# Kernel optimization log

Measured on AMD Instinct MI355X. Metric: run time of the kernel, lower is better.

## Reference

```python
import jax, jax.numpy as jnp
import numpy as np

B, T, C, H, F = 4, 1024, 1024, 16, 4096
D = C // H

def _ln(x, g, b):
    m = x.mean(-1, keepdims=True)
    v = ((x - m) ** 2).mean(-1, keepdims=True)
    return (x - m) * jax.lax.rsqrt(v + 1e-5) * g + b

def setup_inputs() -> dict:
    key = jax.random.key(0)
    ks = jax.random.split(key, 9)
    p = lambda k, shape: jax.random.normal(k, shape, jnp.float32) * 0.02
    return dict(
        x=jax.random.normal(ks[0], (B, T, C), jnp.float32),
        context=jax.random.normal(ks[1], (B, T, C), jnp.float32),
        ln1_g=jnp.ones((C,), jnp.float32), ln1_b=jnp.zeros((C,), jnp.float32),
        qkv_w=p(ks[2], (C, 3 * C)), qkv_b=jnp.zeros((3 * C,), jnp.float32),
        attn_out_w=p(ks[3], (C, C)), attn_out_b=jnp.zeros((C,), jnp.float32),
        lnc_g=jnp.ones((C,), jnp.float32), lnc_b=jnp.zeros((C,), jnp.float32),
        q_w=p(ks[4], (C, C)), q_b=jnp.zeros((C,), jnp.float32),
        kv_w=p(ks[5], (C, 2 * C)), kv_b=jnp.zeros((2 * C,), jnp.float32),
        cross_out_w=p(ks[6], (C, C)), cross_out_b=jnp.zeros((C,), jnp.float32),
        ln2_g=jnp.ones((C,), jnp.float32), ln2_b=jnp.zeros((C,), jnp.float32),
        ffn_w1=p(ks[7], (C, F)), ffn_b1=jnp.zeros((F,), jnp.float32),
        ffn_w2=p(ks[8], (F, C)), ffn_b2=jnp.zeros((C,), jnp.float32),
    )

def reference(x, context, ln1_g, ln1_b, qkv_w, qkv_b, attn_out_w, attn_out_b,
              lnc_g, lnc_b, q_w, q_b, kv_w, kv_b, cross_out_w, cross_out_b,
              ln2_g, ln2_b, ffn_w1, ffn_b1, ffn_w2, ffn_b2):
    scale = 1.0 / np.sqrt(D)
    # --- causal self-attention ---
    h = _ln(x, ln1_g, ln1_b)
    qkv = (h @ qkv_w + qkv_b).reshape(B, T, 3, H, D)
    q, k, v = qkv[:, :, 0], qkv[:, :, 1], qkv[:, :, 2]  # [B,T,H,D]
    s = jnp.einsum('bqhd,bkhd->bhqk', q, k) * scale     # [B,H,T,T]
    causal = jnp.tril(jnp.ones((T, T), bool))
    s = jnp.where(causal, s, -jnp.inf)
    a = jax.nn.softmax(s, axis=-1)
    o = jnp.einsum('bhqk,bkhd->bqhd', a, v).reshape(B, T, C)
    x = x + o @ attn_out_w + attn_out_b
    # --- cross-attention (query=x, context=encoder) ---
    h = _ln(x, lnc_g, lnc_b)
    q = (h @ q_w + q_b).reshape(B, T, H, D)
    kv = (context @ kv_w + kv_b).reshape(B, T, 2, H, D)
    k, v = kv[:, :, 0], kv[:, :, 1]
    s = jnp.einsum('bqhd,bkhd->bhqk', q, k) * scale
    a = jax.nn.softmax(s, axis=-1)
    o = jnp.einsum('bhqk,bkhd->bqhd', a, v).reshape(B, T, C)
    x = x + o @ cross_out_w + cross_out_b
    # --- FFN (exact GELU as in torch default) ---
    h = _ln(x, ln2_g, ln2_b)
    h = jax.nn.gelu(h @ ffn_w1 + ffn_b1, approximate=False)
    return x + h @ ffn_w2 + ffn_b2
```

## Files before the change

### kernel.cpp

```cpp
#include <hip/hip_runtime.h>
#include <hip/hip_bf16.h>

#define BT 4096
#define TT 1024
#define HN 16

typedef __attribute__((ext_vector_type(8))) short bf16x8;
typedef __attribute__((ext_vector_type(4))) float f32x4;

__device__ __forceinline__ unsigned short f2bf(float f) {
    unsigned u = __builtin_bit_cast(unsigned, f);
    unsigned r = (u + 0x7fffu + ((u >> 16) & 1u)) >> 16;
    return (unsigned short)r;
}

__device__ __forceinline__ void g2l16(const void* g, void* l) {
    __builtin_amdgcn_global_load_lds(
        (__attribute__((address_space(1))) void*)(g),
        (__attribute__((address_space(3))) void*)(l), 16, 0, 0);
}

__global__ __launch_bounds__(256)
void transpose_cast(const float* __restrict__ W, unsigned short* __restrict__ Wt,
                    int K, int N)
{
    __shared__ float tile[32][33];
    int n0 = blockIdx.x * 32, k0 = blockIdx.y * 32;
    int tx = threadIdx.x, ty = threadIdx.y;
#pragma unroll
    for (int i = ty; i < 32; i += 8)
        tile[i][tx] = W[(size_t)(k0 + i) * N + n0 + tx];
    __syncthreads();
#pragma unroll
    for (int i = ty; i < 32; i += 8)
        Wt[(size_t)(n0 + i) * K + k0 + tx] = f2bf(tile[tx][i]);
}

__global__ __launch_bounds__(256)
void transpose_v(const unsigned short* __restrict__ v, unsigned short* __restrict__ vt,
                 int stride)
{
    __shared__ unsigned short tile[32][33];
    int d0 = blockIdx.x * 32, t0 = blockIdx.y * 32, bh = blockIdx.z;
    int b = bh >> 4, h = bh & 15;
    int tx = threadIdx.x, ty = threadIdx.y;
#pragma unroll
    for (int i = ty; i < 32; i += 8)
        tile[i][tx] = v[((size_t)b * TT + t0 + i) * stride + h * 64 + d0 + tx];
    __syncthreads();
#pragma unroll
    for (int i = ty; i < 32; i += 8)
        vt[((size_t)bh * 64 + d0 + i) * TT + t0 + tx] = tile[tx][i];
}

__global__ __launch_bounds__(256)
void cast_bf16(const float* __restrict__ in, unsigned short* __restrict__ out)
{
    int i = blockIdx.x * 256 + threadIdx.x;
    float4 v = ((const float4*)in)[i];
    ushort4 o;
    o.x = f2bf(v.x); o.y = f2bf(v.y); o.z = f2bf(v.z); o.w = f2bf(v.w);
    ((ushort4*)out)[i] = o;
}

__global__ __launch_bounds__(256)
void ln_kernel(const float* __restrict__ x, const float* __restrict__ g,
               const float* __restrict__ bta, unsigned short* __restrict__ out)
{
    __shared__ float red[8];
    int row = blockIdx.x;
    const float* xr = x + (size_t)row * 1024;
    float4 v = ((const float4*)xr)[threadIdx.x];
    float s = v.x + v.y + v.z + v.w;
    float q = v.x*v.x + v.y*v.y + v.z*v.z + v.w*v.w;
#pragma unroll
    for (int m = 1; m < 64; m <<= 1) {
        s += __shfl_xor(s, m, 64);
        q += __shfl_xor(q, m, 64);
    }
    int wave = threadIdx.x >> 6;
    if ((threadIdx.x & 63) == 0) { red[wave] = s; red[4 + wave] = q; }
    __syncthreads();
    s = red[0] + red[1] + red[2] + red[3];
    q = red[4] + red[5] + red[6] + red[7];
    float mean = s * (1.f / 1024.f);
    float var  = q * (1.f / 1024.f) - mean * mean;
    float rstd = rsqrtf(var + 1e-5f);
    float4 gv = ((const float4*)g)[threadIdx.x];
    float4 bv = ((const float4*)bta)[threadIdx.x];
    ushort4 o;
    o.x = f2bf((v.x - mean) * rstd * gv.x + bv.x);
    o.y = f2bf((v.y - mean) * rstd * gv.y + bv.y);
    o.z = f2bf((v.z - mean) * rstd * gv.z + bv.z);
    o.w = f2bf((v.w - mean) * rstd * gv.w + bv.w);
    ((ushort4*)(out + (size_t)row * 1024))[threadIdx.x] = o;
}

template<int MODE>
__global__ __launch_bounds__(256)
void gemm_bt(const unsigned short* __restrict__ A,
             const unsigned short* __restrict__ Bt,
             const float* __restrict__ bias,
             const float* __restrict__ res,
             void* __restrict__ outp,
             int M, int N, int K)
{
    __shared__ unsigned short lA[128 * 64];
    __shared__ unsigned short lB[128 * 64];
    const int tid = threadIdx.x;
    const int wave = tid >> 6, lane = tid & 63;
    const int quad = lane >> 4, l16 = lane & 15;
    const int m0 = blockIdx.y * 128, n0 = blockIdx.x * 128;
    const int wrow = (wave >> 1) * 64, wcol = (wave & 1) * 64;

    f32x4 acc[4][4];
#pragma unroll
    for (int i = 0; i < 4; ++i)
#pragma unroll
        for (int j = 0; j < 4; ++j)
#pragma unroll
            for (int r = 0; r < 4; ++r) acc[i][j][r] = 0.f;

    for (int k0 = 0; k0 < K; k0 += 64) {
        __syncthreads();
#pragma unroll
        for (int it = 0; it < 4; ++it) {
            int chunk = it * 256 + tid;
            int row = chunk >> 3, kc = chunk & 7;
            g2l16(A  + (size_t)(m0 + row) * K + k0 + kc * 8, &lA[chunk * 8]);
            g2l16(Bt + (size_t)(n0 + row) * K + k0 + kc * 8, &lB[chunk * 8]);
        }
        __syncthreads();
#pragma unroll
        for (int kk = 0; kk < 64; kk += 32) {
            bf16x8 af[4], bfr[4];
#pragma unroll
            for (int i = 0; i < 4; ++i)
                af[i] = *(const bf16x8*)&lA[(wrow + i * 16 + l16) * 64 + kk + quad * 8];
#pragma unroll
            for (int j = 0; j < 4; ++j)
                bfr[j] = *(const bf16x8*)&lB[(wcol + j * 16 + l16) * 64 + kk + quad * 8];
#pragma unroll
            for (int i = 0; i < 4; ++i)
#pragma unroll
                for (int j = 0; j < 4; ++j)
                    acc[i][j] = __builtin_amdgcn_mfma_f32_16x16x32_bf16(af[i], bfr[j], acc[i][j], 0, 0, 0);
        }
    }

#pragma unroll
    for (int i = 0; i < 4; ++i) {
#pragma unroll
        for (int r = 0; r < 4; ++r) {
            int m = m0 + wrow + i * 16 + quad * 4 + r;
#pragma unroll
            for (int j = 0; j < 4; ++j) {
                int n = n0 + wcol + j * 16 + l16;
                float v = acc[i][j][r] + bias[n];
                if (MODE == 1) v = 0.5f * v * (1.f + erff(v * 0.70710678118654752f));
                size_t idx = (size_t)m * N + n;
                if (MODE == 2) ((float*)outp)[idx] = v + res[idx];
                else ((unsigned short*)outp)[idx] = f2bf(v);
            }
        }
    }
}

__global__ __launch_bounds__(256)
void attn_kernel(const unsigned short* __restrict__ qp,
                 const unsigned short* __restrict__ kp,
                 const unsigned short* __restrict__ vt,
                 unsigned short* __restrict__ op,
                 int qstride, int kstride, int causal)
{
    __shared__ unsigned short lK[64 * 72];
    __shared__ unsigned short lV[64 * 72];
    __shared__ unsigned short lP[4][16 * 72];

    const int tid = threadIdx.x;
    const int wave = tid >> 6, lane = tid & 63;
    const int quad = lane >> 4, l16 = lane & 15;
    const int bh = blockIdx.y, b = bh >> 4, h = bh & 15;
    const int qtile = causal ? (gridDim.x - 1 - blockIdx.x) : blockIdx.x;
    const int q0 = qtile * 64;
    const size_t rowbase = (size_t)b * TT;
    const int hoff = h * 64;
    const unsigned short* vbase = vt + (size_t)bh * 64 * TT;

    bf16x8 qf[2];
    {
        int qrow = q0 + wave * 16 + l16;
        const unsigned short* qrp = qp + (rowbase + qrow) * (size_t)qstride + hoff;
        qf[0] = *(const bf16x8*)(qrp + quad * 8);
        qf[1] = *(const bf16x8*)(qrp + 32 + quad * 8);
    }

    f32x4 oacc[4];
#pragma unroll
    for (int jd = 0; jd < 4; ++jd)
#pragma unroll
        for (int r = 0; r < 4; ++r) oacc[jd][r] = 0.f;
    float mrun = -1e30f, lrun = 0.f;

    const int nkt = causal ? (qtile + 1) : (TT / 64);
    for (int kt = 0; kt < nkt; ++kt) {
        __syncthreads();
#pragma unroll
        for (int it = 0; it < 2; ++it) {
            int c = it * 256 + tid;
            int r8 = c >> 3, cc = c & 7;
            *(bf16x8*)&lK[r8 * 72 + cc * 8] =
                *(const bf16x8*)(kp + (rowbase + kt * 64 + r8) * (size_t)kstride + hoff + cc * 8);
            *(bf16x8*)&lV[r8 * 72 + cc * 8] =
                *(const bf16x8*)(vbase + (size_t)r8 * TT + kt * 64 + cc * 8);
        }
        __syncthreads();

        f32x4 s[4];
#pragma unroll
        for (int i = 0; i < 4; ++i)
#pragma unroll
            for (int r = 0; r < 4; ++r) s[i][r] = 0.f;
#pragma unroll
        for (int kk = 0; kk < 2; ++kk) {
            bf16x8 kf[4];
#pragma unroll
            for (int i = 0; i < 4; ++i)
                kf[i] = *(const bf16x8*)&lK[(i * 16 + l16) * 72 + kk * 32 + quad * 8];
#pragma unroll
            for (int i = 0; i < 4; ++i)
                s[i] = __builtin_amdgcn_mfma_f32_16x16x32_bf16(kf[i], qf[kk], s[i], 0, 0, 0);
        }

        const int qg = q0 + wave * 16 + l16;
        const bool domask = (causal != 0) && (kt == qtile);
        float mloc = -1e30f;
#pragma unroll
        for (int i = 0; i < 4; ++i)
#pragma unroll
            for (int r = 0; r < 4; ++r) {
                float v = s[i][r] * 0.125f;
                if (domask) {
                    int kg = kt * 64 + i * 16 + quad * 4 + r;
                    if (kg > qg) v = -1e30f;
                }
                s[i][r] = v;
                mloc = fmaxf(mloc, v);
            }
        mloc = fmaxf(mloc, __shfl_xor(mloc, 16, 64));
        mloc = fmaxf(mloc, __shfl_xor(mloc, 32, 64));
        float mn = fmaxf(mrun, mloc);
        float alpha = __expf(mrun - mn);
        mrun = mn;
        float ls = 0.f;
#pragma unroll
        for (int i = 0; i < 4; ++i)
#pragma unroll
            for (int r = 0; r < 4; ++r) {
                float p = __expf(s[i][r] - mn);
                s[i][r] = p;
                ls += p;
            }
        ls += __shfl_xor(ls, 16, 64);
        ls += __shfl_xor(ls, 32, 64);
        lrun = lrun * alpha + ls;

        float arow[4];
#pragma unroll
        for (int r = 0; r < 4; ++r)
            arow[r] = __shfl(alpha, quad * 4 + r, 64);
#pragma unroll
        for (int jd = 0; jd < 4; ++jd)
#pragma unroll
            for (int r = 0; r < 4; ++r) oacc[jd][r] *= arow[r];

        unsigned short* pw = lP[wave];
#pragma unroll
        for (int i = 0; i < 4; ++i) {
            ushort4 pk;
            pk.x = f2bf(s[i][0]); pk.y = f2bf(s[i][1]);
            pk.z = f2bf(s[i][2]); pk.w = f2bf(s[i][3]);
            *(ushort4*)&pw[l16 * 72 + i * 16 + quad * 4] = pk;
        }

#pragma unroll
        for (int kk = 0; kk < 2; ++kk) {
            bf16x8 pf = *(const bf16x8*)&pw[l16 * 72 + kk * 32 + quad * 8];
            bf16x8 vf[4];
#pragma unroll
            for (int jd = 0; jd < 4; ++jd)
                vf[jd] = *(const bf16x8*)&lV[(jd * 16 + l16) * 72 + kk * 32 + quad * 8];
#pragma unroll
            for (int jd = 0; jd < 4; ++jd)
                oacc[jd] = __builtin_amdgcn_mfma_f32_16x16x32_bf16(pf, vf[jd], oacc[jd], 0, 0, 0);
        }
    }

    float ir[4];
#pragma unroll
    for (int r = 0; r < 4; ++r)
        ir[r] = 1.f / __shfl(lrun, quad * 4 + r, 64);
#pragma unroll
    for (int r = 0; r < 4; ++r) {
        int qg = q0 + wave * 16 + quad * 4 + r;
        unsigned short* orow = op + (rowbase + qg) * (size_t)1024 + hoff;
#pragma unroll
        for (int jd = 0; jd < 4; ++jd)
            orow[jd * 16 + l16] = f2bf(oacc[jd][r] * ir[r]);
    }
}

extern "C" void kernel_launch(void* const* d_in, const int* in_sizes, int n_in,
                              void* d_out, int out_size, void* d_ws, size_t ws_size,
                              hipStream_t stream)
{
    const float* x     = (const float*)d_in[0];
    const float* ctx   = (const float*)d_in[1];
    const float* ln1_g = (const float*)d_in[2];
    const float* ln1_b = (const float*)d_in[3];
    const float* qkv_w = (const float*)d_in[4];
    const float* qkv_b = (const float*)d_in[5];
    const float* aow   = (const float*)d_in[6];
    const float* aob   = (const float*)d_in[7];
    const float* lnc_g = (const float*)d_in[8];
    const float* lnc_b = (const float*)d_in[9];
    const float* q_w   = (const float*)d_in[10];
    const float* q_b   = (const float*)d_in[11];
    const float* kv_w  = (const float*)d_in[12];
    const float* kv_b  = (const float*)d_in[13];
    const float* cow   = (const float*)d_in[14];
    const float* cob   = (const float*)d_in[15];
    const float* ln2_g = (const float*)d_in[16];
    const float* ln2_b = (const float*)d_in[17];
    const float* f1w   = (const float*)d_in[18];
    const float* f1b   = (const float*)d_in[19];
    const float* f2w   = (const float*)d_in[20];
    const float* f2b   = (const float*)d_in[21];

    char* ws = (char*)d_ws;
    size_t off = 0;
    auto alloc = [&](size_t bytes) {
        char* p = ws + off;
        off += (bytes + 255) & ~(size_t)255;
        return p;
    };

    unsigned short* WtQKV = (unsigned short*)alloc((size_t)3072 * 1024 * 2);
    unsigned short* WtAO  = (unsigned short*)alloc((size_t)1024 * 1024 * 2);
    unsigned short* WtQ   = (unsigned short*)alloc((size_t)1024 * 1024 * 2);
    unsigned short* WtKV  = (unsigned short*)alloc((size_t)2048 * 1024 * 2);
    unsigned short* WtCO  = (unsigned short*)alloc((size_t)1024 * 1024 * 2);
    unsigned short* WtF1  = (unsigned short*)alloc((size_t)4096 * 1024 * 2);
    unsigned short* WtF2  = (unsigned short*)alloc((size_t)1024 * 4096 * 2);
    unsigned short* hA    = (unsigned short*)alloc((size_t)BT * 1024 * 2);
    unsigned short* ctxb  = (unsigned short*)alloc((size_t)BT * 1024 * 2);
    unsigned short* qkvb  = (unsigned short*)alloc((size_t)BT * 3072 * 2);
    unsigned short* o1    = (unsigned short*)alloc((size_t)BT * 1024 * 2);
    float*          x1    = (float*)alloc((size_t)BT * 1024 * 4);
    unsigned short* qb    = (unsigned short*)alloc((size_t)BT * 1024 * 2);
    unsigned short* kvb   = (unsigned short*)alloc((size_t)BT * 2048 * 2);
    unsigned short* o2    = (unsigned short*)alloc((size_t)BT * 1024 * 2);
    float*          x2    = (float*)alloc((size_t)BT * 1024 * 4);
    unsigned short* mid   = (unsigned short*)alloc((size_t)BT * 4096 * 2);
    unsigned short* vT1   = (unsigned short*)alloc((size_t)BT * 1024 * 2);
    unsigned short* vT2   = (unsigned short*)alloc((size_t)BT * 1024 * 2);

    dim3 tb(32, 8);
    transpose_cast<<<dim3(3072/32, 1024/32), tb, 0, stream>>>(qkv_w, WtQKV, 1024, 3072);
    transpose_cast<<<dim3(1024/32, 1024/32), tb, 0, stream>>>(aow,   WtAO,  1024, 1024);
    transpose_cast<<<dim3(1024/32, 1024/32), tb, 0, stream>>>(q_w,   WtQ,   1024, 1024);
    transpose_cast<<<dim3(2048/32, 1024/32), tb, 0, stream>>>(kv_w,  WtKV,  1024, 2048);
    transpose_cast<<<dim3(1024/32, 1024/32), tb, 0, stream>>>(cow,   WtCO,  1024, 1024);
    transpose_cast<<<dim3(4096/32, 1024/32), tb, 0, stream>>>(f1w,   WtF1,  1024, 4096);
    transpose_cast<<<dim3(1024/32, 4096/32), tb, 0, stream>>>(f2w,   WtF2,  4096, 1024);

    cast_bf16<<<BT * 1024 / 4 / 256, 256, 0, stream>>>(ctx, ctxb);

    ln_kernel<<<BT, 256, 0, stream>>>(x, ln1_g, ln1_b, hA);
    gemm_bt<0><<<dim3(3072/128, BT/128), 256, 0, stream>>>(hA, WtQKV, qkv_b, nullptr, qkvb, BT, 3072, 1024);
    transpose_v<<<dim3(2, TT/32, 64), tb, 0, stream>>>(qkvb + 2048, vT1, 3072);
    attn_kernel<<<dim3(TT/64, 64), 256, 0, stream>>>(qkvb, qkvb + 1024, vT1, o1, 3072, 3072, 1);
    gemm_bt<2><<<dim3(1024/128, BT/128), 256, 0, stream>>>(o1, WtAO, aob, x, x1, BT, 1024, 1024);

    ln_kernel<<<BT, 256, 0, stream>>>(x1, lnc_g, lnc_b, hA);
    gemm_bt<0><<<dim3(1024/128, BT/128), 256, 0, stream>>>(hA, WtQ, q_b, nullptr, qb, BT, 1024, 1024);
    gemm_bt<0><<<dim3(2048/128, BT/128), 256, 0, stream>>>(ctxb, WtKV, kv_b, nullptr, kvb, BT, 2048, 1024);
    transpose_v<<<dim3(2, TT/32, 64), tb, 0, stream>>>(kvb + 1024, vT2, 2048);
    attn_kernel<<<dim3(TT/64, 64), 256, 0, stream>>>(qb, kvb, vT2, o2, 1024, 2048, 0);
    gemm_bt<2><<<dim3(1024/128, BT/128), 256, 0, stream>>>(o2, WtCO, cob, x1, x2, BT, 1024, 1024);

    ln_kernel<<<BT, 256, 0, stream>>>(x2, ln2_g, ln2_b, hA);
    gemm_bt<1><<<dim3(4096/128, BT/128), 256, 0, stream>>>(hA, WtF1, f1b, nullptr, mid, BT, 4096, 1024);
    gemm_bt<2><<<dim3(1024/128, BT/128), 256, 0, stream>>>(mid, WtF2, f2b, x2, (float*)d_out, BT, 1024, 4096);
}
```

Before: 620.2 us.

## Batch weight transposes, merge Q/KV GEMMs, add split-K and smaller-tile GEMMs

Replaces seven weight transpose launches with one table-driven kernel. Merges the cross-attention Q and KV projections into a single dual-GEMM launch. Uses 64-row tiles for the N=1024 output projections so the grid has more blocks. Splits the K=4096 FFN down-projection four ways into fp32 partials, reusing the qkv scratch region, then sums them with bias and residual in a separate reduction kernel. Together these aim to raise CU utilisation on undersized grids and cut launch overhead, at the cost of extra partial-sum memory traffic and reliance on the allocator placing the scratch buffers contiguously.

```diff
diff --git a/kernel.cpp b/kernel.cpp
--- a/kernel.cpp
+++ b/kernel.cpp
@@ -20,12 +20,28 @@
         (__attribute__((address_space(3))) void*)(l), 16, 0, 0);
 }
 
-__global__ __launch_bounds__(256)
-void transpose_cast(const float* __restrict__ W, unsigned short* __restrict__ Wt,
-                    int K, int N)
+struct TransJobs {
+    const float* W[7];
+    unsigned short* Wt[7];
+    int K[7], N[7];
+    int start[8];
+};
+
+__global__ __launch_bounds__(256)
+void transpose_all(TransJobs J)
 {
     __shared__ float tile[32][33];
-    int n0 = blockIdx.x * 32, k0 = blockIdx.y * 32;
+    int bx = blockIdx.x;
+    int j = 0;
+#pragma unroll
+    for (int t = 0; t < 7; ++t)
+        if (bx >= J.start[t + 1]) j = t + 1;
+    int t = bx - J.start[j];
+    int K = J.K[j], N = J.N[j];
+    int ntx = N >> 5;
+    int n0 = (t % ntx) * 32, k0 = (t / ntx) * 32;
+    const float* W = J.W[j];
+    unsigned short* Wt = J.Wt[j];
     int tx = threadIdx.x, ty = threadIdx.y;
 #pragma unroll
     for (int i = ty; i < 32; i += 8)
@@ -97,6 +113,76 @@
 }
 
 template<int MODE>
+__device__ __forceinline__
+void gemm_core(unsigned short* lA, unsigned short* lB,
+               const unsigned short* __restrict__ A,
+               const unsigned short* __restrict__ Bt,
+               const float* __restrict__ bias,
+               const float* __restrict__ res,
+               void* __restrict__ outp,
+               int N, int K, int m0, int n0, int kbeg, int kend)
+{
+    const int tid = threadIdx.x;
+    const int wave = tid >> 6, lane = tid & 63;
+    const int quad = lane >> 4, l16 = lane & 15;
+    const int wrow = (wave >> 1) * 64, wcol = (wave & 1) * 64;
+
+    f32x4 acc[4][4];
+#pragma unroll
+    for (int i = 0; i < 4; ++i)
+#pragma unroll
+        for (int j = 0; j < 4; ++j)
+#pragma unroll
+            for (int r = 0; r < 4; ++r) acc[i][j][r] = 0.f;
+
+    for (int k0 = kbeg; k0 < kend; k0 += 64) {
+        __syncthreads();
+#pragma unroll
+        for (int it = 0; it < 4; ++it) {
+            int chunk = it * 256 + tid;
+            int row = chunk >> 3, kc = chunk & 7;
+            g2l16(A  + (size_t)(m0 + row) * K + k0 + kc * 8, &lA[chunk * 8]);
+            g2l16(Bt + (size_t)(n0 + row) * K + k0 + kc * 8, &lB[chunk * 8]);
+        }
+        __syncthreads();
+#pragma unroll
+        for (int kk = 0; kk < 64; kk += 32) {
+            bf16x8 af[4], bfr[4];
+#pragma unroll
+            for (int i = 0; i < 4; ++i)
+                af[i] = *(const bf16x8*)&lA[(wrow + i * 16 + l16) * 64 + kk + quad * 8];
+#pragma unroll
+            for (int j = 0; j < 4; ++j)
+                bfr[j] = *(const bf16x8*)&lB[(wcol + j * 16 + l16) * 64 + kk + quad * 8];
+#pragma unroll
+            for (int i = 0; i < 4; ++i)
+#pragma unroll
+                for (int j = 0; j < 4; ++j)
+                    acc[i][j] = __builtin_amdgcn_mfma_f32_16x16x32_bf16(af[i], bfr[j], acc[i][j], 0, 0, 0);
+        }
+    }
+
+#pragma unroll
+    for (int i = 0; i < 4; ++i) {
+#pragma unroll
+        for (int r = 0; r < 4; ++r) {
+            int m = m0 + wrow + i * 16 + quad * 4 + r;
+#pragma unroll
+            for (int j = 0; j < 4; ++j) {
+                int n = n0 + wcol + j * 16 + l16;
+                float v = acc[i][j][r];
+                if (MODE != 3) v += bias[n];
+                if (MODE == 1) v = 0.5f * v * (1.f + erff(v * 0.70710678118654752f));
+                size_t idx = (size_t)m * N + n;
+                if (MODE == 2) ((float*)outp)[idx] = v + res[idx];
+                else if (MODE == 3) ((float*)outp)[idx] = v;
+                else ((unsigned short*)outp)[idx] = f2bf(v);
+            }
+        }
+    }
+}
+
+template<int MODE>
 __global__ __launch_bounds__(256)
 void gemm_bt(const unsigned short* __restrict__ A,
              const unsigned short* __restrict__ Bt,
@@ -107,15 +193,80 @@
 {
     __shared__ unsigned short lA[128 * 64];
     __shared__ unsigned short lB[128 * 64];
+    gemm_core<MODE>(lA, lB, A, Bt, bias, res, outp, N, K,
+                    blockIdx.y * 128, blockIdx.x * 128, 0, K);
+}
+
+__global__ __launch_bounds__(256)
+void gemm_dual(const unsigned short* __restrict__ A1, const unsigned short* __restrict__ B1,
+               const float* __restrict__ b1, unsigned short* __restrict__ o1p, int N1, int nbx1,
+               const unsigned short* __restrict__ A2, const unsigned short* __restrict__ B2,
+               const float* __restrict__ b2, unsigned short* __restrict__ o2p, int N2,
+               int K)
+{
+    __shared__ unsigned short lA[128 * 64];
+    __shared__ unsigned short lB[128 * 64];
+    int bx = blockIdx.x;
+    if (bx < nbx1)
+        gemm_core<0>(lA, lB, A1, B1, b1, nullptr, o1p, N1, K,
+                     blockIdx.y * 128, bx * 128, 0, K);
+    else
+        gemm_core<0>(lA, lB, A2, B2, b2, nullptr, o2p, N2, K,
+                     blockIdx.y * 128, (bx - nbx1) * 128, 0, K);
+}
+
+__global__ __launch_bounds__(256)
+void gemm_splitk(const unsigned short* __restrict__ A,
+                 const unsigned short* __restrict__ Bt,
+                 float* __restrict__ part,
+                 int M, int N, int K, int kslice)
+{
+    __shared__ unsigned short lA[128 * 64];
+    __shared__ unsigned short lB[128 * 64];
+    int kz = blockIdx.z;
+    gemm_core<3>(lA, lB, A, Bt, nullptr, nullptr,
+                 part + (size_t)kz * M * N, N, K,
+                 blockIdx.y * 128, blockIdx.x * 128,
+                 kz * kslice, (kz + 1) * kslice);
+}
+
+__global__ __launch_bounds__(256)
+void reduce4(const float* __restrict__ part, const float* __restrict__ bias,
+             const float* __restrict__ res, float* __restrict__ out, int MN)
+{
+    int i = blockIdx.x * 256 + threadIdx.x;
+    const float4* p = (const float4*)part;
+    int q = MN >> 2;
+    float4 a = p[i], b = p[i + q], c = p[i + 2 * q], d = p[i + 3 * q];
+    float4 bs = ((const float4*)bias)[i & 255];
+    float4 rr = ((const float4*)res)[i];
+    float4 o;
+    o.x = a.x + b.x + c.x + d.x + bs.x + rr.x;
+    o.y = a.y + b.y + c.y + d.y + bs.y + rr.y;
+    o.z = a.z + b.z + c.z + d.z + bs.z + rr.z;
+    o.w = a.w + b.w + c.w + d.w + bs.w + rr.w;
+    ((float4*)out)[i] = o;
+}
+
+__global__ __launch_bounds__(256)
+void gemm_small2(const unsigned short* __restrict__ A,
+                 const unsigned short* __restrict__ Bt,
+                 const float* __restrict__ bias,
+                 const float* __restrict__ res,
+                 float* __restrict__ outp,
+                 int M, int N, int K)
+{
+    __shared__ unsigned short lA[64 * 64];
+    __shared__ unsigned short lB[128 * 64];
     const int tid = threadIdx.x;
     const int wave = tid >> 6, lane = tid & 63;
     const int quad = lane >> 4, l16 = lane & 15;
-    const int m0 = blockIdx.y * 128, n0 = blockIdx.x * 128;
-    const int wrow = (wave >> 1) * 64, wcol = (wave & 1) * 64;
-
-    f32x4 acc[4][4];
-#pragma unroll
-    for (int i = 0; i < 4; ++i)
+    const int m0 = blockIdx.y * 64, n0 = blockIdx.x * 128;
+    const int wrow = (wave >> 1) * 32, wcol = (wave & 1) * 64;
+
+    f32x4 acc[2][4];
+#pragma unroll
+    for (int i = 0; i < 2; ++i)
 #pragma unroll
         for (int j = 0; j < 4; ++j)
 #pragma unroll
@@ -124,24 +275,29 @@
     for (int k0 = 0; k0 < K; k0 += 64) {
         __syncthreads();
 #pragma unroll
-        for (int it = 0; it < 4; ++it) {
+        for (int it = 0; it < 6; ++it) {
             int chunk = it * 256 + tid;
-            int row = chunk >> 3, kc = chunk & 7;
-            g2l16(A  + (size_t)(m0 + row) * K + k0 + kc * 8, &lA[chunk * 8]);
-            g2l16(Bt + (size_t)(n0 + row) * K + k0 + kc * 8, &lB[chunk * 8]);
+            if (chunk < 512) {
+                int row = chunk >> 3, kc = chunk & 7;
+                g2l16(A + (size_t)(m0 + row) * K + k0 + kc * 8, &lA[chunk * 8]);
+            } else {
+                int cb = chunk - 512;
+                int row = cb >> 3, kc = cb & 7;
+                g2l16(Bt + (size_t)(n0 + row) * K + k0 + kc * 8, &lB[cb * 8]);
+            }
         }
         __syncthreads();
 #pragma unroll
         for (int kk = 0; kk < 64; kk += 32) {
-            bf16x8 af[4], bfr[4];
-#pragma unroll
-            for (int i = 0; i < 4; ++i)
+            bf16x8 af[2], bfr[4];
+#pragma unroll
+            for (int i = 0; i < 2; ++i)
                 af[i] = *(const bf16x8*)&lA[(wrow + i * 16 + l16) * 64 + kk + quad * 8];
 #pragma unroll
             for (int j = 0; j < 4; ++j)
                 bfr[j] = *(const bf16x8*)&lB[(wcol + j * 16 + l16) * 64 + kk + quad * 8];
 #pragma unroll
-            for (int i = 0; i < 4; ++i)
+            for (int i = 0; i < 2; ++i)
 #pragma unroll
                 for (int j = 0; j < 4; ++j)
                     acc[i][j] = __builtin_amdgcn_mfma_f32_16x16x32_bf16(af[i], bfr[j], acc[i][j], 0, 0, 0);
@@ -149,18 +305,15 @@
     }
 
 #pragma unroll
-    for (int i = 0; i < 4; ++i) {
+    for (int i = 0; i < 2; ++i) {
 #pragma unroll
         for (int r = 0; r < 4; ++r) {
             int m = m0 + wrow + i * 16 + quad * 4 + r;
 #pragma unroll
             for (int j = 0; j < 4; ++j) {
                 int n = n0 + wcol + j * 16 + l16;
-                float v = acc[i][j][r] + bias[n];
-                if (MODE == 1) v = 0.5f * v * (1.f + erff(v * 0.70710678118654752f));
                 size_t idx = (size_t)m * N + n;
-                if (MODE == 2) ((float*)outp)[idx] = v + res[idx];
-                else ((unsigned short*)outp)[idx] = f2bf(v);
+                outp[idx] = acc[i][j][r] + bias[n] + res[idx];
             }
         }
     }
@@ -365,31 +518,43 @@
     unsigned short* vT1   = (unsigned short*)alloc((size_t)BT * 1024 * 2);
     unsigned short* vT2   = (unsigned short*)alloc((size_t)BT * 1024 * 2);
 
+    float* partials = (float*)qkvb;
+
+    TransJobs J;
+    J.W[0]=qkv_w; J.Wt[0]=WtQKV; J.K[0]=1024; J.N[0]=3072;
+    J.W[1]=aow;   J.Wt[1]=WtAO;  J.K[1]=1024; J.N[1]=1024;
+    J.W[2]=q_w;   J.Wt[2]=WtQ;   J.K[2]=1024; J.N[2]=1024;
+    J.W[3]=kv_w;  J.Wt[3]=WtKV;  J.K[3]=1024; J.N[3]=2048;
+    J.W[4]=cow;   J.Wt[4]=WtCO;  J.K[4]=1024; J.N[4]=1024;
+    J.W[5]=f1w;   J.Wt[5]=WtF1;  J.K[5]=1024; J.N[5]=4096;
+    J.W[6]=f2w;   J.Wt[6]=WtF2;  J.K[6]=4096; J.N[6]=1024;
+    int acc = 0;
+    for (int j = 0; j < 7; ++j) {
+        J.start[j] = acc;
+        acc += (J.N[j] / 32) * (J.K[j] / 32);
+    }
+    J.start[7] = acc;
+
     dim3 tb(32, 8);
-    transpose_cast<<<dim3(3072/32, 1024/32), tb, 0, stream>>>(qkv_w, WtQKV, 1024, 3072);
-    transpose_cast<<<dim3(1024/32, 1024/32), tb, 0, stream>>>(aow,   WtAO,  1024, 1024);
-    transpose_cast<<<dim3(1024/32, 1024/32), tb, 0, stream>>>(q_w,   WtQ,   1024, 1024);
-    transpose_cast<<<dim3(2048/32, 1024/32), tb, 0, stream>>>(kv_w,  WtKV,  1024, 2048);
-    transpose_cast<<<dim3(1024/32, 1024/32), tb, 0, stream>>>(cow,   WtCO,  1024, 1024);
-    transpose_cast<<<dim3(4096/32, 1024/32), tb, 0, stream>>>(f1w,   WtF1,  1024, 4096);
-    transpose_cast<<<dim3(1024/32, 4096/32), tb, 0, stream>>>(f2w,   WtF2,  4096, 1024);
-
+    transpose_all<<<acc, tb, 0, stream>>>(J);
     cast_bf16<<<BT * 1024 / 4 / 256, 256, 0, stream>>>(ctx, ctxb);
 
     ln_kernel<<<BT, 256, 0, stream>>>(x, ln1_g, ln1_b, hA);
     gemm_bt<0><<<dim3(3072/128, BT/128), 256, 0, stream>>>(hA, WtQKV, qkv_b, nullptr, qkvb, BT, 3072, 1024);
     transpose_v<<<dim3(2, TT/32, 64), tb, 0, stream>>>(qkvb + 2048, vT1, 3072);
     attn_kernel<<<dim3(TT/64, 64), 256, 0, stream>>>(qkvb, qkvb + 1024, vT1, o1, 3072, 3072, 1);
-    gemm_bt<2><<<dim3(1024/128, BT/128), 256, 0, stream>>>(o1, WtAO, aob, x, x1, BT, 1024, 1024);
+    gemm_small2<<<dim3(1024/128, BT/64), 256, 0, stream>>>(o1, WtAO, aob, x, x1, BT, 1024, 1024);
 
     ln_kernel<<<BT, 256, 0, stream>>>(x1, lnc_g, lnc_b, hA);
-    gemm_bt<0><<<dim3(1024/128, BT/128), 256, 0, stream>>>(hA, WtQ, q_b, nullptr, qb, BT, 1024, 1024);
-    gemm_bt<0><<<dim3(2048/128, BT/128), 256, 0, stream>>>(ctxb, WtKV, kv_b, nullptr, kvb, BT, 2048, 1024);
+    gemm_dual<<<dim3(1024/128 + 2048/128, BT/128), 256, 0, stream>>>(
+        hA, WtQ, q_b, qb, 1024, 1024/128,
+        ctxb, WtKV, kv_b, kvb, 2048, 1024);
     transpose_v<<<dim3(2, TT/32, 64), tb, 0, stream>>>(kvb + 1024, vT2, 2048);
     attn_kernel<<<dim3(TT/64, 64), 256, 0, stream>>>(qb, kvb, vT2, o2, 1024, 2048, 0);
-    gemm_bt<2><<<dim3(1024/128, BT/128), 256, 0, stream>>>(o2, WtCO, cob, x1, x2, BT, 1024, 1024);
+    gemm_small2<<<dim3(1024/128, BT/64), 256, 0, stream>>>(o2, WtCO, cob, x1, x2, BT, 1024, 1024);
 
     ln_kernel<<<BT, 256, 0, stream>>>(x2, ln2_g, ln2_b, hA);
     gemm_bt<1><<<dim3(4096/128, BT/128), 256, 0, stream>>>(hA, WtF1, f1b, nullptr, mid, BT, 4096, 1024);
-    gemm_bt<2><<<dim3(1024/128, BT/128), 256, 0, stream>>>(mid, WtF2, f2b, x2, (float*)d_out, BT, 1024, 4096);
-}
+    gemm_splitk<<<dim3(1024/128, BT/128, 4), 256, 0, stream>>>(mid, WtF2, partials, BT, 1024, 4096, 1024);
+    reduce4<<<BT * 1024 / 4 / 256, 256, 0, stream>>>(partials, f2b, x2, (float*)d_out, BT * 1024);
+}
```

Result: faster. 585.9 us (-5.5%).
